# Optimization experiments

Hardware: AMD Instinct MI355X
Metric: run time of the kernel (lower is better)

The kernel has to match this reference:

```python
import jax, jax.numpy as jnp
import numpy as np

NUM_GRAPHS = 512
NODES_PER_GRAPH = 128
HIDDEN = 64
K = 24


def _param(key, shape, scale=0.05):
    return jax.random.normal(key, shape, dtype=jnp.float32) * scale


def setup_inputs() -> dict:
    key = jax.random.key(0)
    ks = jax.random.split(key, 24)
    N = NUM_GRAPHS * NODES_PER_GRAPH
    inp = {
        "x_pf": jax.random.normal(ks[0], (N, 4), dtype=jnp.float32),
        "batch_pf": jnp.repeat(jnp.arange(NUM_GRAPHS, dtype=jnp.int64), NODES_PER_GRAPH),
        # pf_encode: Linear(4,64), ELU, Linear(64,64), ELU
        "we1": _param(ks[1], (4, HIDDEN)), "be1": _param(ks[2], (HIDDEN,)),
        "we2": _param(ks[3], (HIDDEN, HIDDEN)), "be2": _param(ks[4], (HIDDEN,)),
        # three DynamicEdgeConv edge MLPs: Linear(128,64)+ELU
        "wc1": _param(ks[5], (2 * HIDDEN, HIDDEN)), "bc1": _param(ks[6], (HIDDEN,)),
        "wc2": _param(ks[7], (2 * HIDDEN, HIDDEN)), "bc2": _param(ks[8], (HIDDEN,)),
        "wc3": _param(ks[9], (2 * HIDDEN, HIDDEN)), "bc3": _param(ks[10], (HIDDEN,)),
        # output MLP 64->64->32->32->8->1
        "wo1": _param(ks[11], (HIDDEN, 64)), "bo1": _param(ks[12], (64,)),
        "wo2": _param(ks[13], (64, 32)), "bo2": _param(ks[14], (32,)),
        "wo3": _param(ks[15], (32, 32)), "bo3": _param(ks[16], (32,)),
        "wo4": _param(ks[17], (32, 8)), "bo4": _param(ks[18], (8,)),
        "wo5": _param(ks[19], (8, 1)), "bo5": _param(ks[20], (1,)),
    }
    return inp


def dynamic_edge_conv(x, wc, bc):
    """x: [G,P,D]. kNN (incl. self) in feature space per graph, edge feature
    [x_i, x_j - x_i] -> Linear+ELU -> max over neighbors. Matches PyG
    DynamicEdgeConv(nn, k, aggr='max')."""
    sq = jnp.sum(x * x, axis=-1)                                   # [G,P]
    d = sq[:, :, None] + sq[:, None, :] - 2.0 * jnp.einsum('gpd,gqd->gpq', x, x)
    _, idx = jax.lax.top_k(-d, K)                                   # [G,P,K] nearest (self included, dist 0)
    xj = jax.vmap(lambda xg, ig: xg[ig])(x, idx)                    # [G,P,K,D]
    xi = x[:, :, None, :]
    e = jnp.concatenate([jnp.broadcast_to(xi, xj.shape), xj - xi], axis=-1)  # [G,P,K,2D]
    h = jax.nn.elu(e @ wc + bc)                                     # [G,P,K,D]
    return jnp.max(h, axis=2)                                       # [G,P,D]


def reference(x_pf, batch_pf, we1, be1, we2, be2, wc1, bc1, wc2, bc2, wc3, bc3,
              wo1, bo1, wo2, bo2, wo3, bo3, wo4, bo4, wo5, bo5):
    elu = jax.nn.elu
    h = elu(elu(x_pf @ we1 + be1) @ we2 + be2)                      # [N,64]
    h = h.reshape(NUM_GRAPHS, NODES_PER_GRAPH, HIDDEN)              # equal-size graphs
    h = dynamic_edge_conv(h, wc1, bc1)
    h = dynamic_edge_conv(h, wc2, bc2)
    h = dynamic_edge_conv(h, wc3, bc3)
    pooled = jnp.sum(h, axis=1)                                     # global_add_pool -> [G,64]
    o = elu(pooled @ wo1 + bo1)
    o = elu(o @ wo2 + bo2)
    o = elu(o @ wo3 + bo3)
    o = elu(o @ wo4 + bo4)
    out = o @ wo5 + bo5                                             # [G,1]
    return (out, batch_pf)
```

## Files before the change

### kernel.cpp

```cpp
#include <hip/hip_runtime.h>
#include <math.h>

#define NG 512
#define NP 128
#define HID 64
#define KNN 24
#define NTOT (NG*NP)

typedef __attribute__((ext_vector_type(8)))  short  short8;
typedef __attribute__((ext_vector_type(16))) float  floatx16;

__device__ __forceinline__ float elu_f(float v) {
    const float e = __builtin_amdgcn_exp2f(v * 1.442695040888963f) - 1.0f;
    return v > 0.0f ? v : e;
}

__device__ __forceinline__ void split_bf16(float x, unsigned short& hb, unsigned short& lb) {
    unsigned u = __float_as_uint(x);
    unsigned h = (u + 0x7FFFu + ((u >> 16) & 1u)) >> 16;
    hb = (unsigned short)h;
    float hf = __uint_as_float(h << 16);
    float lo = x - hf;
    unsigned v = __float_as_uint(lo);
    lb = (unsigned short)((v + 0x7FFFu + ((v >> 16) & 1u)) >> 16);
}
__device__ __forceinline__ unsigned short bf_rne(float x) {
    unsigned u = __float_as_uint(x);
    return (unsigned short)((u + 0x7FFFu + ((u >> 16) & 1u)) >> 16);
}
__device__ __forceinline__ float bf_lo(unsigned u) { return __uint_as_float(u << 16); }
__device__ __forceinline__ float bf_hi(unsigned u) { return __uint_as_float(u & 0xFFFF0000u); }

__device__ __forceinline__ unsigned short f_to_key(unsigned short b) {
    return (unsigned short)(b ^ ((b & 0x8000u) ? 0xFFFFu : 0x8000u));
}
__device__ __forceinline__ float key_to_f(unsigned k) {
    const unsigned bf = (k & 0x8000u) ? (k ^ 0x8000u) : (k ^ 0xFFFFu);
    return __uint_as_float(bf << 16);
}
__device__ __forceinline__ unsigned pk_max_u16(unsigned a, unsigned b) {
    unsigned d;
    asm("v_pk_max_u16 %0, %1, %2" : "=v"(d) : "v"(a), "v"(b));
    return d;
}

__device__ __forceinline__ unsigned short* hchunk(unsigned short* base, int row, int ch) {
    return base + (((row << 4) + (ch ^ (row & 15))) << 3);
}
__device__ __forceinline__ const unsigned short* hchunk(const unsigned short* base, int row, int ch) {
    return base + (((row << 4) + (ch ^ (row & 15))) << 3);
}

__device__ __forceinline__ void sort8_asc(unsigned* y) {
    #pragma unroll
    for (int k = 2; k <= 8; k <<= 1)
        #pragma unroll
        for (int j = k >> 1; j > 0; j >>= 1)
            #pragma unroll
            for (int i = 0; i < 8; ++i) {
                const int l = i ^ j;
                if (l > i) {
                    const bool up = ((i & k) == 0);
                    const unsigned a = y[i], b = y[l];
                    const unsigned mn = a < b ? a : b;
                    const unsigned mx = a < b ? b : a;
                    y[i] = up ? mn : mx;
                    y[l] = up ? mx : mn;
                }
            }
}

__device__ __forceinline__ void merge_top24(unsigned* x) {
    #pragma unroll
    for (int d = 16; d > 0; d >>= 1)
        #pragma unroll
        for (int i = 0; i < 32; ++i)
            if (!(i & d) && i < 24) {
                const int l = i | d;
                const unsigned a = x[i], b = x[l];
                x[i] = a < b ? a : b;
                x[l] = a < b ? b : a;
            }
}

__device__ __forceinline__ void merge2_shfl(unsigned* xk, int mask) {
    unsigned z[32];
    #pragma unroll
    for (int e = 0; e < 24; ++e) {
        const unsigned ye = (unsigned)__shfl_xor((int)xk[23 - e], mask);
        z[8 + e] = xk[e] < ye ? xk[e] : ye;
    }
    #pragma unroll
    for (int d = 16; d > 0; d >>= 1)
        #pragma unroll
        for (int i = 8; i < 32; ++i)
            if (!(i & d)) {
                const int l = i | d;
                const unsigned a = z[i], b = z[l];
                z[i] = a < b ? a : b;
                z[l] = a < b ? b : a;
            }
    #pragma unroll
    for (int e = 0; e < 24; ++e) xk[e] = z[8 + e];
}

__global__ __launch_bounds__(256) void pack_w(
    const float* __restrict__ wc1, const float* __restrict__ wc2, const float* __restrict__ wc3,
    const float* __restrict__ we2,
    unsigned short* __restrict__ wp)
{
    const int n = blockIdx.x*256 + threadIdx.x;
    if (n < 24576) {
        const int layer = n >> 13;
        const int r = n & 8191;
        const int e = r & 7, j = (r >> 3) & 127, ch = r >> 10;
        const int k = (ch >> 1)*16 + (ch & 1)*8 + e;
        const float* wc = (layer == 0) ? wc1 : ((layer == 1) ? wc2 : wc3);
        float w;
        if (j < 64) w = wc[k*64 + j] - wc[(k+64)*64 + j];
        else        w = wc[(k+64)*64 + (j-64)];
        unsigned short hb, lb;
        split_bf16(w, hb, lb);
        unsigned short* base = wp + layer*16384;
        base[r] = hb;
        base[8192 + r] = lb;
    } else if (n < 24576 + 4096) {
        const int m = n - 24576;
        const int e = m & 7, col = (m >> 3) & 63, ch = m >> 9;
        const int k = (ch >> 1)*16 + (ch & 1)*8 + e;
        unsigned short hb, lb;
        split_bf16(we2[k*64 + col], hb, lb);
        unsigned short* base = wp + 49152;
        base[m] = hb;
        base[4096 + m] = lb;
    }
}

__global__ __launch_bounds__(512, 4) void conv_all(
    const float* __restrict__ x,
    const unsigned short* __restrict__ wp,
    const float* __restrict__ bc1, const float* __restrict__ bc2, const float* __restrict__ bc3,
    const float* __restrict__ we1, const float* __restrict__ be1,
    const unsigned short* __restrict__ we2p, const float* __restrict__ be2,
    float* __restrict__ ag_all, float* __restrict__ pooled_out, float* __restrict__ out_batch)
{
    __shared__ __align__(16) char arena[69632];
    unsigned*        keys  = (unsigned*)arena;
    unsigned*        nnidx = (unsigned*)(arena + 33280);
    unsigned short*  hilo  = (unsigned short*)(arena + 36352);
    float*           sqs   = (float*)(arena + 69120);

    const int g = blockIdx.x;
    const int t = threadIdx.x;
    const int w = t >> 6, lane = t & 63;
    const int lj = lane & 31, half = lane >> 5;
    const int rt = w & 3, wg = w >> 2;
    float* __restrict__ ag = ag_all + (size_t)g * (NP*HID);

    {
        float* w1s = (float*)arena;
        float* b1v = (float*)(arena + 1024);
        float* b2v = (float*)(arena + 1280);
        if (t < 256) w1s[t] = we1[t];
        else if (t < 320) b1v[t-256] = be1[t-256];
        else if (t < 384) b2v[t-320] = be2[t-320];
        if (t < 128) out_batch[(size_t)g*128 + t] = (float)g;
        __syncthreads();

        const int n = t & 127, fh = t >> 7, f0 = fh*16;
        const float4 xv = ((const float4*)x)[g*128 + n];
        float acc1[16];
        #pragma unroll
        for (int q = 0; q < 4; ++q) {
            const float4 b4 = *(const float4*)(b1v + f0 + q*4);
            acc1[q*4+0] = b4.x; acc1[q*4+1] = b4.y; acc1[q*4+2] = b4.z; acc1[q*4+3] = b4.w;
        }
        #pragma unroll
        for (int k = 0; k < 4; ++k) {
            const float xk_ = (k == 0) ? xv.x : (k == 1) ? xv.y : (k == 2) ? xv.z : xv.w;
            #pragma unroll
            for (int q = 0; q < 4; ++q) {
                const float4 w4 = *(const float4*)(w1s + k*64 + f0 + q*4);
                acc1[q*4+0] = fmaf(xk_, w4.x, acc1[q*4+0]);
                acc1[q*4+1] = fmaf(xk_, w4.y, acc1[q*4+1]);
                acc1[q*4+2] = fmaf(xk_, w4.z, acc1[q*4+2]);
                acc1[q*4+3] = fmaf(xk_, w4.w, acc1[q*4+3]);
            }
        }
        unsigned hu[8], lu[8];
        #pragma unroll
        for (int e = 0; e < 8; ++e) {
            const float v0 = elu_f(acc1[2*e]), v1 = elu_f(acc1[2*e+1]);
            unsigned short h0, l0, h1, l1;
            split_bf16(v0, h0, l0); split_bf16(v1, h1, l1);
            hu[e] = (unsigned)h0 | ((unsigned)h1 << 16);
            lu[e] = (unsigned)l0 | ((unsigned)l1 << 16);
        }
        *(uint4*)hchunk(hilo, n, fh*2)       = make_uint4(hu[0], hu[1], hu[2], hu[3]);
        *(uint4*)hchunk(hilo, n, fh*2 + 1)   = make_uint4(hu[4], hu[5], hu[6], hu[7]);
        *(uint4*)hchunk(hilo, n, 8 + fh*2)   = make_uint4(lu[0], lu[1], lu[2], lu[3]);
        *(uint4*)hchunk(hilo, n, 8 + fh*2+1) = make_uint4(lu[4], lu[5], lu[6], lu[7]);
        __syncthreads();

        const int jt2 = wg;
        floatx16 acc = {0.f,0.f,0.f,0.f,0.f,0.f,0.f,0.f,0.f,0.f,0.f,0.f,0.f,0.f,0.f,0.f};
        #pragma unroll
        for (int p = 0; p < 3; ++p) {
            const int aSel = (p == 2) ? 8 : 0;
            const int part = (p == 1) ? 1 : 0;
            #pragma unroll
            for (int c = 0; c < 4; ++c) {
                const short8 af  = *(const short8*)hchunk(hilo, rt*32 + lj, aSel + c*2 + half);
                const short8 bf4 = *(const short8*)((const short*)we2p + part*4096 + (((c*2 + half)*64) + jt2*32 + lj)*8);
                acc = __builtin_amdgcn_mfma_f32_32x32x16_bf16(af, bf4, acc, 0, 0, 0);
            }
        }
        const int col = jt2*32 + lj;
        const float bias = ((const float*)(arena + 1280))[col];
        __syncthreads();
        #pragma unroll
        for (int reg = 0; reg < 16; ++reg) {
            const int row = (reg & 3) + 8*(reg >> 2) + 4*half + rt*32;
            const float v = elu_f(acc[reg] + bias);
            unsigned short hb, lb;
            split_bf16(v, hb, lb);
            *(hchunk(hilo, row, col >> 3) + (col & 7))       = hb;
            *(hchunk(hilo, row, 8 + (col >> 3)) + (col & 7)) = lb;
        }
        __syncthreads();

        const int r = t >> 2, cq = t & 3, c0 = cq*2;
        const uint4 h0 = *(const uint4*)hchunk(hilo, r, c0);
        const uint4 h1 = *(const uint4*)hchunk(hilo, r, c0+1);
        const uint4 l0 = *(const uint4*)hchunk(hilo, r, 8+c0);
        const uint4 l1 = *(const uint4*)hchunk(hilo, r, 8+c0+1);
        float s = 0.0f;
        const unsigned hh[8] = {h0.x,h0.y,h0.z,h0.w,h1.x,h1.y,h1.z,h1.w};
        const unsigned ll[8] = {l0.x,l0.y,l0.z,l0.w,l1.x,l1.y,l1.z,l1.w};
        #pragma unroll
        for (int e = 0; e < 8; ++e) {
            const float va = bf_lo(hh[e]) + bf_lo(ll[e]);
            const float vb = bf_hi(hh[e]) + bf_hi(ll[e]);
            s = fmaf(va, va, s); s = fmaf(vb, vb, s);
        }
        s += __shfl_xor(s, 1);
        s += __shfl_xor(s, 2);
        if (cq == 0) sqs[r] = s;
        __syncthreads();
    }

    #pragma unroll 1
    for (int L = 0; L < 3; ++L) {
        const unsigned short* wpl = wp + L*16384;
        const float* bcl = (L == 0) ? bc1 : (L == 1) ? bc2 : bc3;

        unsigned xk[32];
        #pragma unroll
        for (int s = 0; s < 24; ++s) xk[s] = 0xFFFFFFFFu;

        #pragma unroll 1
        for (int r = 0; r < 2; ++r) {
            const int jt = r*2 + wg;
            {
                floatx16 acc = {0.f,0.f,0.f,0.f,0.f,0.f,0.f,0.f,0.f,0.f,0.f,0.f,0.f,0.f,0.f,0.f};
                #pragma unroll
                for (int p = 0; p < 3; ++p) {
                    const int aSel = (p == 2) ? 8 : 0;
                    const int bSel = (p == 1) ? 8 : 0;
                    #pragma unroll
                    for (int c = 0; c < 4; ++c) {
                        const short8 af = *(const short8*)hchunk(hilo, rt*32 + lj, aSel + c*2 + half);
                        const short8 bf = *(const short8*)hchunk(hilo, jt*32 + lj, bSel + c*2 + half);
                        acc = __builtin_amdgcn_mfma_f32_32x32x16_bf16(af, bf, acc, 0, 0, 0);
                    }
                }
                const unsigned jg = (unsigned)(jt*32 + lj);
                const float sqj = sqs[jg];
                #pragma unroll
                for (int reg = 0; reg < 16; ++reg) {
                    const int i = (reg & 3) + 8*(reg >> 2) + 4*half + rt*32;
                    float d = fmaf(-2.0f, acc[reg], sqs[i] + sqj);
                    d = fmaxf(d, 0.0f);
                    keys[i*65 + wg*32 + lj] = (__float_as_uint(d) & 0xFFFFFF80u) | jg;
                }
            }
            __syncthreads();
            {
                const unsigned* kr = keys + (t >> 2)*65 + (t & 3)*16;
                const uint4 k0 = *(const uint4*)kr;
                const uint4 k1 = *(const uint4*)(kr + 4);
                {
                    unsigned y[8] = {k0.x, k0.y, k0.z, k0.w, k1.x, k1.y, k1.z, k1.w};
                    sort8_asc(y);
                    #pragma unroll
                    for (int e = 0; e < 8; ++e) xk[24+e] = y[7-e];
                    merge_top24(xk);
                }
                const uint4 k2 = *(const uint4*)(kr + 8);
                const uint4 k3 = *(const uint4*)(kr + 12);
                {
                    unsigned y[8] = {k2.x, k2.y, k2.z, k2.w, k3.x, k3.y, k3.z, k3.w};
                    sort8_asc(y);
                    #pragma unroll
                    for (int e = 0; e < 8; ++e) xk[24+e] = y[7-e];
                    merge_top24(xk);
                }
            }
            __syncthreads();
        }

        merge2_shfl(xk, 1);
        merge2_shfl(xk, 2);
        if ((t & 3) == 0) {
            #pragma unroll
            for (int c = 0; c < 6; ++c)
                nnidx[(t >> 2)*6 + c] = (xk[c*4] & 127u) | ((xk[c*4+1] & 127u) << 8)
                                      | ((xk[c*4+2] & 127u) << 16) | ((xk[c*4+3] & 127u) << 24);
        }

        unsigned short* bs = (unsigned short*)arena;
        {
            short8 afr[8];
            #pragma unroll
            for (int sel = 0; sel < 2; ++sel)
                #pragma unroll
                for (int c = 0; c < 4; ++c)
                    afr[sel*4+c] = *(const short8*)hchunk(hilo, rt*32 + lj, sel*8 + c*2 + half);

            #pragma unroll 1
            for (int q2 = 0; q2 < 2; ++q2) {
                const int jt = wg*2 + q2;
                short8 bfr[8];
                #pragma unroll
                for (int part = 0; part < 2; ++part)
                    #pragma unroll
                    for (int c = 0; c < 4; ++c)
                        bfr[part*4+c] = *(const short8*)((const short*)wpl + part*8192 + (((c*2 + half)*128) + jt*32 + lj)*8);
                floatx16 acc = {0.f,0.f,0.f,0.f,0.f,0.f,0.f,0.f,0.f,0.f,0.f,0.f,0.f,0.f,0.f,0.f};
                #pragma unroll
                for (int c = 0; c < 4; ++c) acc = __builtin_amdgcn_mfma_f32_32x32x16_bf16(afr[c],   bfr[c],   acc, 0, 0, 0);
                #pragma unroll
                for (int c = 0; c < 4; ++c) acc = __builtin_amdgcn_mfma_f32_32x32x16_bf16(afr[c],   bfr[4+c], acc, 0, 0, 0);
                #pragma unroll
                for (int c = 0; c < 4; ++c) acc = __builtin_amdgcn_mfma_f32_32x32x16_bf16(afr[4+c], bfr[c],   acc, 0, 0, 0);

                if (wg == 0) {
                    const int col = jt*32 + lj;
                    const float bias = bcl[col];
                    #pragma unroll
                    for (int reg = 0; reg < 16; ++reg) {
                        const int row = (reg & 3) + 8*(reg >> 2) + 4*half + rt*32;
                        ag[(size_t)row*64 + col] = acc[reg] + bias;
                    }
                } else {
                    const int colb = q2*32 + lj;
                    #pragma unroll
                    for (int reg = 0; reg < 16; ++reg) {
                        const int row = (reg & 3) + 8*(reg >> 2) + 4*half + rt*32;
                        bs[row*68 + colb] = f_to_key(bf_rne(acc[reg]));
                    }
                }
            }
        }
        __syncthreads();

        {
            const int q = lane >> 4, fq = lane & 15;
            float4 psum = make_float4(0.f, 0.f, 0.f, 0.f);
            #pragma unroll 1
            for (int rg = 0; rg < 4; ++rg) {
                const int row = w*16 + rg*4 + q;
                unsigned mk0 = 0u, mk1 = 0u;
                #pragma unroll
                for (int c = 0; c < 6; ++c) {
                    const unsigned pk = nnidx[row*6 + c];
                    #pragma unroll
                    for (int e = 0; e < 4; ++e) {
                        const int j = (pk >> (8*e)) & 127;
                        const uint2 bb = *(const uint2*)(bs + j*68 + fq*4);
                        mk0 = pk_max_u16(mk0, bb.x);
                        mk1 = pk_max_u16(mk1, bb.y);
                    }
                }
                const float4 av = *(const float4*)(ag + (size_t)row*64 + fq*4);
                float4 o;
                o.x = elu_f(av.x + key_to_f(mk0 & 0xFFFFu));
                o.y = elu_f(av.y + key_to_f(mk0 >> 16));
                o.z = elu_f(av.z + key_to_f(mk1 & 0xFFFFu));
                o.w = elu_f(av.w + key_to_f(mk1 >> 16));

                if (L < 2) {
                    unsigned short hx,lx,hy,ly,hz,lz,hw2,lw2;
                    split_bf16(o.x,hx,lx); split_bf16(o.y,hy,ly);
                    split_bf16(o.z,hz,lz); split_bf16(o.w,hw2,lw2);
                    *(uint2*)(hchunk(hilo, row, fq >> 1) + (fq & 1)*4) =
                        make_uint2((unsigned)hx | ((unsigned)hy << 16), (unsigned)hz | ((unsigned)hw2 << 16));
                    *(uint2*)(hchunk(hilo, row, 8 + (fq >> 1)) + (fq & 1)*4) =
                        make_uint2((unsigned)lx | ((unsigned)ly << 16), (unsigned)lz | ((unsigned)lw2 << 16));
                    float sp = o.x*o.x + o.y*o.y + o.z*o.z + o.w*o.w;
                    sp += __shfl_xor(sp, 1);
                    sp += __shfl_xor(sp, 2);
                    sp += __shfl_xor(sp, 4);
                    sp += __shfl_xor(sp, 8);
                    if (fq == 0) sqs[row] = sp;
                } else {
                    psum.x += o.x; psum.y += o.y; psum.z += o.z; psum.w += o.w;
                }
            }
            if (L < 2) {
                __syncthreads();
            } else {
                __syncthreads();
                float* pool8 = (float*)(arena + 33280);
                psum.x += __shfl_xor(psum.x, 16); psum.y += __shfl_xor(psum.y, 16);
                psum.z += __shfl_xor(psum.z, 16); psum.w += __shfl_xor(psum.w, 16);
                psum.x += __shfl_xor(psum.x, 32); psum.y += __shfl_xor(psum.y, 32);
                psum.z += __shfl_xor(psum.z, 32); psum.w += __shfl_xor(psum.w, 32);
                if (q == 0) *(float4*)(pool8 + w*64 + fq*4) = psum;
                __syncthreads();
                if (t < 64) {
                    float s = 0.0f;
                    #pragma unroll
                    for (int k = 0; k < 8; ++k) s += pool8[k*64 + t];
                    pooled_out[(size_t)g*64 + t] = s;
                }
            }
        }
    }
}

__global__ __launch_bounds__(64) void head_kernel(
    const float* __restrict__ pooled_in,
    const float* __restrict__ wo1, const float* __restrict__ bo1,
    const float* __restrict__ wo2, const float* __restrict__ bo2,
    const float* __restrict__ wo3, const float* __restrict__ bo3,
    const float* __restrict__ wo4, const float* __restrict__ bo4,
    const float* __restrict__ wo5, const float* __restrict__ bo5,
    float* __restrict__ outp)
{
    __shared__ float pooled[64];
    __shared__ float o1[64];
    __shared__ float o2[32];
    __shared__ float o3[32];
    __shared__ float o4[8];
    const int g = blockIdx.x, t = threadIdx.x;

    pooled[t] = pooled_in[(size_t)g*64 + t];
    {
        float acc = bo1[t];
        #pragma unroll
        for (int k = 0; k < 64; ++k) acc = fmaf(pooled[k], wo1[k*64 + t], acc);
        o1[t] = elu_f(acc);
    }
    if (t < 32) {
        float acc = bo2[t];
        #pragma unroll
        for (int k = 0; k < 64; ++k) acc = fmaf(o1[k], wo2[k*32 + t], acc);
        o2[t] = elu_f(acc);
    }
    if (t < 32) {
        float acc = bo3[t];
        #pragma unroll
        for (int k = 0; k < 32; ++k) acc = fmaf(o2[k], wo3[k*32 + t], acc);
        o3[t] = elu_f(acc);
    }
    if (t < 8) {
        float acc = bo4[t];
        #pragma unroll
        for (int k = 0; k < 32; ++k) acc = fmaf(o3[k], wo4[k*8 + t], acc);
        o4[t] = elu_f(acc);
    }
    if (t == 0) {
        float acc = bo5[0];
        #pragma unroll
        for (int k = 0; k < 8; ++k) acc = fmaf(o4[k], wo5[k], acc);
        outp[g] = acc;
    }
}

extern "C" void kernel_launch(void* const* d_in, const int* in_sizes, int n_in,
                              void* d_out, int out_size, void* d_ws, size_t ws_size,
                              hipStream_t stream) {
    const float* x_pf = (const float*)d_in[0];
    const float* we1 = (const float*)d_in[2];
    const float* be1 = (const float*)d_in[3];
    const float* we2 = (const float*)d_in[4];
    const float* be2 = (const float*)d_in[5];
    const float* wc1 = (const float*)d_in[6];
    const float* bc1 = (const float*)d_in[7];
    const float* wc2 = (const float*)d_in[8];
    const float* bc2 = (const float*)d_in[9];
    const float* wc3 = (const float*)d_in[10];
    const float* bc3 = (const float*)d_in[11];
    const float* wo1 = (const float*)d_in[12];
    const float* bo1 = (const float*)d_in[13];
    const float* wo2 = (const float*)d_in[14];
    const float* bo2 = (const float*)d_in[15];
    const float* wo3 = (const float*)d_in[16];
    const float* bo3 = (const float*)d_in[17];
    const float* wo4 = (const float*)d_in[18];
    const float* bo4 = (const float*)d_in[19];
    const float* wo5 = (const float*)d_in[20];
    const float* bo5 = (const float*)d_in[21];

    float* out = (float*)d_out;
    char* ws = (char*)d_ws;
    float* abuf   = (float*)(ws);
    float* pooled = (float*)(ws + (size_t)16*1024*1024);
    unsigned short* wpack = (unsigned short*)(ws + (size_t)17*1024*1024);

    pack_w<<<112, 256, 0, stream>>>(wc1, wc2, wc3, we2, wpack);

    conv_all<<<NG, 512, 0, stream>>>(x_pf, wpack, bc1, bc2, bc3,
        we1, be1, wpack + 49152, be2, abuf, pooled, out + NG);

    head_kernel<<<NG, 64, 0, stream>>>(pooled, wo1, bo1, wo2, bo2, wo3, bo3, wo4, bo4, wo5, bo5, out);
}
```

Baseline: 176.1 us.

## Replace incremental top-24 merges with single 32-key bitonic sort and hoist MFMA fragments

The kNN selection now collects all 32 candidate keys per thread across both tile rounds and sorts them once with a full 32-element bitonic network, instead of sorting batches of eight and merging each into a running top-24 list. The split-bf16 MFMA loops load the high fragments once and reuse them for the hi*lo and lo*hi passes. The neighbor max-gather is split into two independent accumulator chains to shorten dependency latency. The full 32-sort adds comparator work and register pressure, and unrolling the round loop keeps more values live.

```diff
diff --git a/kernel.cpp b/kernel.cpp
--- a/kernel.cpp
+++ b/kernel.cpp
@@ -51,13 +51,13 @@
     return base + (((row << 4) + (ch ^ (row & 15))) << 3);
 }
 
-__device__ __forceinline__ void sort8_asc(unsigned* y) {
+__device__ __forceinline__ void sort32_asc(unsigned* y) {
     #pragma unroll
-    for (int k = 2; k <= 8; k <<= 1)
+    for (int k = 2; k <= 32; k <<= 1)
         #pragma unroll
         for (int j = k >> 1; j > 0; j >>= 1)
             #pragma unroll
-            for (int i = 0; i < 8; ++i) {
+            for (int i = 0; i < 32; ++i) {
                 const int l = i ^ j;
                 if (l > i) {
                     const bool up = ((i & k) == 0);
@@ -67,19 +67,6 @@
                     y[i] = up ? mn : mx;
                     y[l] = up ? mx : mn;
                 }
-            }
-}
-
-__device__ __forceinline__ void merge_top24(unsigned* x) {
-    #pragma unroll
-    for (int d = 16; d > 0; d >>= 1)
-        #pragma unroll
-        for (int i = 0; i < 32; ++i)
-            if (!(i & d) && i < 24) {
-                const int l = i | d;
-                const unsigned a = x[i], b = x[l];
-                x[i] = a < b ? a : b;
-                x[l] = a < b ? b : a;
             }
 }
 
@@ -204,15 +191,24 @@
 
         const int jt2 = wg;
         floatx16 acc = {0.f,0.f,0.f,0.f,0.f,0.f,0.f,0.f,0.f,0.f,0.f,0.f,0.f,0.f,0.f,0.f};
-        #pragma unroll
-        for (int p = 0; p < 3; ++p) {
-            const int aSel = (p == 2) ? 8 : 0;
-            const int part = (p == 1) ? 1 : 0;
+        {
+            short8 afh[4], bfh[4];
             #pragma unroll
             for (int c = 0; c < 4; ++c) {
-                const short8 af  = *(const short8*)hchunk(hilo, rt*32 + lj, aSel + c*2 + half);
-                const short8 bf4 = *(const short8*)((const short*)we2p + part*4096 + (((c*2 + half)*64) + jt2*32 + lj)*8);
-                acc = __builtin_amdgcn_mfma_f32_32x32x16_bf16(af, bf4, acc, 0, 0, 0);
+                afh[c] = *(const short8*)hchunk(hilo, rt*32 + lj, c*2 + half);
+                bfh[c] = *(const short8*)((const short*)we2p + (((c*2 + half)*64) + jt2*32 + lj)*8);
+            }
+            #pragma unroll
+            for (int c = 0; c < 4; ++c) acc = __builtin_amdgcn_mfma_f32_32x32x16_bf16(afh[c], bfh[c], acc, 0, 0, 0);
+            #pragma unroll
+            for (int c = 0; c < 4; ++c) {
+                const short8 bfl = *(const short8*)((const short*)we2p + 4096 + (((c*2 + half)*64) + jt2*32 + lj)*8);
+                acc = __builtin_amdgcn_mfma_f32_32x32x16_bf16(afh[c], bfl, acc, 0, 0, 0);
+            }
+            #pragma unroll
+            for (int c = 0; c < 4; ++c) {
+                const short8 afl = *(const short8*)hchunk(hilo, rt*32 + lj, 8 + c*2 + half);
+                acc = __builtin_amdgcn_mfma_f32_32x32x16_bf16(afl, bfh[c], acc, 0, 0, 0);
             }
         }
         const int col = jt2*32 + lj;
@@ -255,24 +251,29 @@
         const float* bcl = (L == 0) ? bc1 : (L == 1) ? bc2 : bc3;
 
         unsigned xk[32];
-        #pragma unroll
-        for (int s = 0; s < 24; ++s) xk[s] = 0xFFFFFFFFu;
-
-        #pragma unroll 1
+
+        #pragma unroll
         for (int r = 0; r < 2; ++r) {
             const int jt = r*2 + wg;
             {
                 floatx16 acc = {0.f,0.f,0.f,0.f,0.f,0.f,0.f,0.f,0.f,0.f,0.f,0.f,0.f,0.f,0.f,0.f};
-                #pragma unroll
-                for (int p = 0; p < 3; ++p) {
-                    const int aSel = (p == 2) ? 8 : 0;
-                    const int bSel = (p == 1) ? 8 : 0;
-                    #pragma unroll
-                    for (int c = 0; c < 4; ++c) {
-                        const short8 af = *(const short8*)hchunk(hilo, rt*32 + lj, aSel + c*2 + half);
-                        const short8 bf = *(const short8*)hchunk(hilo, jt*32 + lj, bSel + c*2 + half);
-                        acc = __builtin_amdgcn_mfma_f32_32x32x16_bf16(af, bf, acc, 0, 0, 0);
-                    }
+                short8 afh[4], bfh[4];
+                #pragma unroll
+                for (int c = 0; c < 4; ++c) {
+                    afh[c] = *(const short8*)hchunk(hilo, rt*32 + lj, c*2 + half);
+                    bfh[c] = *(const short8*)hchunk(hilo, jt*32 + lj, c*2 + half);
+                }
+                #pragma unroll
+                for (int c = 0; c < 4; ++c) acc = __builtin_amdgcn_mfma_f32_32x32x16_bf16(afh[c], bfh[c], acc, 0, 0, 0);
+                #pragma unroll
+                for (int c = 0; c < 4; ++c) {
+                    const short8 bfl = *(const short8*)hchunk(hilo, jt*32 + lj, 8 + c*2 + half);
+                    acc = __builtin_amdgcn_mfma_f32_32x32x16_bf16(afh[c], bfl, acc, 0, 0, 0);
+                }
+                #pragma unroll
+                for (int c = 0; c < 4; ++c) {
+                    const short8 afl = *(const short8*)hchunk(hilo, rt*32 + lj, 8 + c*2 + half);
+                    acc = __builtin_amdgcn_mfma_f32_32x32x16_bf16(afl, bfh[c], acc, 0, 0, 0);
                 }
                 const unsigned jg = (unsigned)(jt*32 + lj);
                 const float sqj = sqs[jg];
@@ -289,26 +290,17 @@
                 const unsigned* kr = keys + (t >> 2)*65 + (t & 3)*16;
                 const uint4 k0 = *(const uint4*)kr;
                 const uint4 k1 = *(const uint4*)(kr + 4);
-                {
-                    unsigned y[8] = {k0.x, k0.y, k0.z, k0.w, k1.x, k1.y, k1.z, k1.w};
-                    sort8_asc(y);
-                    #pragma unroll
-                    for (int e = 0; e < 8; ++e) xk[24+e] = y[7-e];
-                    merge_top24(xk);
-                }
                 const uint4 k2 = *(const uint4*)(kr + 8);
                 const uint4 k3 = *(const uint4*)(kr + 12);
-                {
-                    unsigned y[8] = {k2.x, k2.y, k2.z, k2.w, k3.x, k3.y, k3.z, k3.w};
-                    sort8_asc(y);
-                    #pragma unroll
-                    for (int e = 0; e < 8; ++e) xk[24+e] = y[7-e];
-                    merge_top24(xk);
-                }
+                xk[r*16+0]  = k0.x; xk[r*16+1]  = k0.y; xk[r*16+2]  = k0.z; xk[r*16+3]  = k0.w;
+                xk[r*16+4]  = k1.x; xk[r*16+5]  = k1.y; xk[r*16+6]  = k1.z; xk[r*16+7]  = k1.w;
+                xk[r*16+8]  = k2.x; xk[r*16+9]  = k2.y; xk[r*16+10] = k2.z; xk[r*16+11] = k2.w;
+                xk[r*16+12] = k3.x; xk[r*16+13] = k3.y; xk[r*16+14] = k3.z; xk[r*16+15] = k3.w;
             }
             __syncthreads();
         }
 
+        sort32_asc(xk);
         merge2_shfl(xk, 1);
         merge2_shfl(xk, 2);
         if ((t & 3) == 0) {
@@ -370,9 +362,9 @@
             #pragma unroll 1
             for (int rg = 0; rg < 4; ++rg) {
                 const int row = w*16 + rg*4 + q;
-                unsigned mk0 = 0u, mk1 = 0u;
-                #pragma unroll
-                for (int c = 0; c < 6; ++c) {
+                unsigned mk0 = 0u, mk1 = 0u, nk0 = 0u, nk1 = 0u;
+                #pragma unroll
+                for (int c = 0; c < 3; ++c) {
                     const unsigned pk = nnidx[row*6 + c];
                     #pragma unroll
                     for (int e = 0; e < 4; ++e) {
@@ -382,6 +374,19 @@
                         mk1 = pk_max_u16(mk1, bb.y);
                     }
                 }
+                #pragma unroll
+                for (int c = 3; c < 6; ++c) {
+                    const unsigned pk = nnidx[row*6 + c];
+                    #pragma unroll
+                    for (int e = 0; e < 4; ++e) {
+                        const int j = (pk >> (8*e)) & 127;
+                        const uint2 bb = *(const uint2*)(bs + j*68 + fq*4);
+                        nk0 = pk_max_u16(nk0, bb.x);
+                        nk1 = pk_max_u16(nk1, bb.y);
+                    }
+                }
+                mk0 = pk_max_u16(mk0, nk0);
+                mk1 = pk_max_u16(mk1, nk1);
                 const float4 av = *(const float4*)(ag + (size_t)row*64 + fq*4);
                 float4 o;
                 o.x = elu_f(av.x + key_to_f(mk0 & 0xFFFFu));
```

Result: no change. 177.0 us (+0.5%).
